# Kernel optimization log

Hardware: AMD Instinct MI355X
Metric: run time of the kernel (lower is better)

The kernel has to match this reference:

```python
import jax, jax.numpy as jnp
import numpy as np

# dims
N, NPG, E, D, ED = 32768, 256, 262144, 128, 32   # nodes, nodes/graph, edges, hidden, edge_dim
HG, CG = 4, 32                                    # GAT heads, per-head channels (HG*CG == D)
HA = 8                                            # global attention heads
DH = D // HA


def _glorot(key, shape):
    fan_in, fan_out = shape[0], shape[-1]
    lim = (6.0 / (fan_in + fan_out)) ** 0.5
    return jax.random.uniform(key, shape, jnp.float32, -lim, lim)


def _ln(x, g, b, eps=1e-5):
    m = x.mean(-1, keepdims=True)
    v = ((x - m) ** 2).mean(-1, keepdims=True)
    return (x - m) * jax.lax.rsqrt(v + eps) * g + b


def setup_inputs() -> dict:
    key = jax.random.key(0)
    ks = jax.random.split(key, 32)
    x = jax.random.normal(ks[0], (N, D), jnp.float32)
    src = jax.random.randint(ks[1], (E,), 0, N, jnp.int32)
    # keep edges intra-graph (graphs are contiguous blocks of NPG nodes)
    dst = (src // NPG) * NPG + jax.random.randint(ks[2], (E,), 0, NPG, jnp.int32)
    edge_index = jnp.stack([src, dst])
    edge_attr = jax.random.normal(ks[3], (E, ED), jnp.float32)
    batch = (jnp.arange(N, dtype=jnp.int32) // NPG)
    return {
        "x": x, "edge_attr": edge_attr,
        # EdgeAwareGATv2 params
        "W_src": _glorot(ks[4], (D, HG * CG)), "W_dst": _glorot(ks[5], (D, HG * CG)),
        "W_edge": _glorot(ks[6], (ED, HG * CG)), "att": _glorot(ks[7], (1, HG, CG)),
        "gat_bias": jnp.zeros((HG * CG,), jnp.float32),
        # GraphMultiHeadAttention params
        "Wq": _glorot(ks[8], (D, D)), "bq": jnp.zeros((D,), jnp.float32),
        "Wk": _glorot(ks[9], (D, D)), "bk": jnp.zeros((D,), jnp.float32),
        "Wv": _glorot(ks[10], (D, D)), "bv": jnp.zeros((D,), jnp.float32),
        "Wo": _glorot(ks[11], (D, D)), "bo": jnp.zeros((D,), jnp.float32),
        "We": _glorot(ks[12], (ED, HA)), "be": jnp.zeros((HA,), jnp.float32),
        # block norms + FFN
        "ln1_g": jnp.ones((D,), jnp.float32), "ln1_b": jnp.zeros((D,), jnp.float32),
        "W1": _glorot(ks[13], (D, 2 * D)), "b1": jnp.zeros((2 * D,), jnp.float32),
        "W2": _glorot(ks[14], (2 * D, D)), "b2": jnp.zeros((D,), jnp.float32),
        "ln2_g": jnp.ones((D,), jnp.float32), "ln2_b": jnp.zeros((D,), jnp.float32),
        "edge_index": edge_index, "batch": batch, "nodes_per_graph": NPG,
    }


def reference(x, edge_attr, W_src, W_dst, W_edge, att, gat_bias,
              Wq, bq, Wk, bk, Wv, bv, Wo, bo, We, be,
              ln1_g, ln1_b, W1, b1, W2, b2, ln2_g, ln2_b,
              edge_index, batch, nodes_per_graph):
    n = int(nodes_per_graph)
    Nn = x.shape[0]
    G = Nn // n
    src, dst = edge_index[0], edge_index[1]

    # ---- local: EdgeAwareGATv2 (segment-softmax attention over incoming edges) ----
    xs = (x @ W_src).reshape(Nn, HG, CG)
    xd = (x @ W_dst).reshape(Nn, HG, CG)
    ef = (edge_attr @ W_edge).reshape(-1, HG, CG)
    msg = jnp.tanh(xs[src] + xd[dst] + ef)                 # [E,HG,CG]
    alpha = (msg * att).sum(-1)                            # [E,HG]
    amax = jax.ops.segment_max(alpha, dst, num_segments=Nn)
    amax = jnp.where(jnp.isfinite(amax), amax, 0.0)        # nodes w/o in-edges
    ex = jnp.exp(alpha - amax[dst])
    den = jax.ops.segment_sum(ex, dst, num_segments=Nn)
    a = ex / (den[dst] + 1e-16)
    h_local = jax.ops.segment_sum(xs[src] * a[:, :, None], dst, num_segments=Nn)
    h_local = h_local.reshape(Nn, HG * CG) + gat_bias

    # ---- global: GraphMultiHeadAttention with edge bias (dense per graph) ----
    q = (x @ Wq + bq).reshape(G, n, HA, DH)
    k = (x @ Wk + bk).reshape(G, n, HA, DH)
    v = (x @ Wv + bv).reshape(G, n, HA, DH)
    attn = jnp.einsum('gnhd,gmhd->gnmh', q, k) * (DH ** -0.5)
    eb = edge_attr @ We + be                               # [E,HA]
    g_id = src // n
    intra = (g_id == dst // n)[:, None]
    attn = attn.at[g_id, src % n, dst % n].add(jnp.where(intra, eb, 0.0))
    attn = jax.nn.softmax(attn, axis=2)                    # softmax over keys (torch dim=1)
    h_attn = jnp.einsum('gnmh,gmhd->gnhd', attn, v).reshape(Nn, D)
    h_attn = h_attn @ Wo + bo

    # ---- GPS combine: residual + norm + FFN ----
    h = _ln(x + h_local + h_attn, ln1_g, ln1_b)
    ffn = jax.nn.gelu(h @ W1 + b1, approximate=False) @ W2 + b2
    return _ln(h + ffn, ln2_g, ln2_b)
```

## Files before the change

### kernel.cpp

```cpp
#include <hip/hip_runtime.h>
#include <hip/hip_bf16.h>

typedef __hip_bfloat16 bf16;
typedef __hip_bfloat162 bf162;
typedef __attribute__((ext_vector_type(8))) short short8;
typedef __attribute__((ext_vector_type(4))) float f32x4;
typedef __attribute__((ext_vector_type(16))) float f32x16;

constexpr int kN   = 32768;
constexpr int kG   = 128;
constexpr int kE   = 262144;
constexpr int kHA  = 8;

__device__ __forceinline__ float b2f(bf16 v){ return __bfloat162float(v); }
__device__ __forceinline__ bf16  f2b(float v){ return __float2bfloat16(v); }
__device__ __forceinline__ float b2f_raw(unsigned short u){
  return __uint_as_float((unsigned)u << 16);
}
__device__ __forceinline__ float tanh_fast(float x){
  float e = __expf(2.f*x);
  return 1.f - 2.f/(e+1.f);
}
__device__ __forceinline__ unsigned int cvtpk_bf16(float lo, float hi){
  unsigned int r;
  asm volatile("v_cvt_pk_bf16_f32 %0, %1, %2" : "=v"(r) : "v"(lo), "v"(hi));
  return r;
}
__device__ __forceinline__ void plane_swap(unsigned int &a, unsigned int &b){
  asm volatile("v_permlane32_swap_b32 %0, %1" : "+v"(a), "+v"(b));
}

__global__ void detect_k(const void* xraw, int* flag){
  const bf16* p = (const bf16*)xraw;
  int good = 0;
  for (int i = threadIdx.x; i < 4096; i += 256){
    float v = fabsf(b2f(p[i]));
    if (v > 0.0009765625f && v < 16.f) good++;
  }
  __shared__ int s[256];
  s[threadIdx.x] = good;
  __syncthreads();
  for (int d = 128; d; d >>= 1){
    if (threadIdx.x < d) s[threadIdx.x] += s[threadIdx.x + d];
    __syncthreads();
  }
  if (threadIdx.x == 0) *flag = (s[0] < 3500) ? 1 : 0;
}

struct ImpEnt { const void* src; void* dst; int n; };
struct ImpArgs { ImpEnt e[23]; };
__global__ __launch_bounds__(256) void import_k(ImpArgs a, const int* __restrict__ flag){
  ImpEnt en = a.e[blockIdx.y];
  const bool f32 = (*flag != 0);
  for (int i = blockIdx.x*256 + threadIdx.x; i < en.n; i += gridDim.x*256){
    float v = f32 ? ((const float*)en.src)[i] : b2f(((const bf16*)en.src)[i]);
    ((float*)en.dst)[i] = v;
  }
}

__global__ __launch_bounds__(256) void repack5_k(const float* __restrict__ W0,
    const float* __restrict__ W1p, const float* __restrict__ W2p,
    const float* __restrict__ W3p, const float* __restrict__ W4p,
    bf16* __restrict__ dst){
  int idx = blockIdx.x*256 + threadIdx.x;
  const float* Ws[5] = {W0, W1p, W2p, W3p, W4p};
  int o = idx >> 14;
  int rem = idx & 16383;
  int j = rem & 7, l = (rem >> 3) & 63, t = rem >> 9;
  int ks = t >> 3, cb = t & 7;
  int k = ks*32 + (l>>4)*8 + j;
  int c = cb*16 + (l&15);
  dst[idx] = f2b(Ws[o][k*128 + c]);
}

struct RepEnt { const float* src; bf16* dst; int total; int ncb_log; int dout; int mode; };
__global__ __launch_bounds__(256) void repack_k(RepEnt e0, RepEnt e1, RepEnt e2,
                                                RepEnt e3, RepEnt e4){
  RepEnt en = (blockIdx.y == 0) ? e0 : (blockIdx.y == 1) ? e1 :
              (blockIdx.y == 2) ? e2 : (blockIdx.y == 3) ? e3 : e4;
  int idx = blockIdx.x*256 + threadIdx.x;
  if (idx >= en.total) return;
  int j = idx & 7, l = (idx >> 3) & 63, t = idx >> 9;
  if (en.mode == 2){
    int k = (l>>4)*8 + j;
    int c = l & 15;
    en.dst[idx] = (c < 8) ? f2b(en.src[k*8 + c]) : f2b(0.f);
    return;
  }
  int ncbm = (1 << en.ncb_log) - 1;
  int ks = t >> en.ncb_log, cb = t & ncbm;
  int k = ks*32 + (l>>4)*8 + j;
  int c = cb*16 + (l&15);
  if (en.mode == 1) c = ((c & 15) << 3) | (c >> 4);
  en.dst[idx] = f2b(en.src[k*en.dout + c]);
}

__global__ __launch_bounds__(256) void gemm5_k(const void* __restrict__ xraw,
    const int* __restrict__ flag,
    const bf16* __restrict__ Wrep, const float* __restrict__ bias5,
    bf16* __restrict__ proj5){
  const int tid = threadIdx.x;
  const int wid = tid >> 6, l = tid & 63;
  const long r0 = (long)blockIdx.x*64 + wid*16;
  const bool f32 = (*flag != 0);
  short8 af[4];
  if (f32){
    const float* fr = (const float*)xraw + (r0 + (l&15))*128;
    #pragma unroll
    for (int ks=0; ks<4; ks++){
      float4 a = *(const float4*)(fr + ks*32 + (l>>4)*8);
      float4 b = *(const float4*)(fr + ks*32 + (l>>4)*8 + 4);
      union{ unsigned int u[4]; short8 s; } c;
      c.u[0]=cvtpk_bf16(a.x,a.y); c.u[1]=cvtpk_bf16(a.z,a.w);
      c.u[2]=cvtpk_bf16(b.x,b.y); c.u[3]=cvtpk_bf16(b.z,b.w);
      af[ks] = c.s;
    }
  } else {
    const short* Arow = (const short*)xraw + (r0 + (l&15))*128;
    #pragma unroll
    for (int ks=0; ks<4; ks++)
      af[ks] = *(const short8*)(Arow + ks*32 + (l>>4)*8);
  }
  const short8* Wp = (const short8*)Wrep;
  const int cc = l & 15, rr = (l >> 4) * 4;
  #pragma unroll 1
  for (int o=0; o<5; o++){
    f32x4 acc[8];
    #pragma unroll
    for (int cb=0; cb<8; cb++) acc[cb] = (f32x4){0.f,0.f,0.f,0.f};
    #pragma unroll
    for (int ks=0; ks<4; ks++){
      #pragma unroll
      for (int cb=0; cb<8; cb++){
        short8 bf = Wp[(o*32 + ks*8 + cb)*64 + l];
        acc[cb] = __builtin_amdgcn_mfma_f32_16x16x32_bf16(af[ks], bf, acc[cb], 0,0,0);
      }
    }
    bf16* outb = proj5 + (long)o*kN*128;
    #pragma unroll
    for (int cb=0; cb<8; cb++){
      float bb = bias5[o*128 + cb*16 + cc];
      #pragma unroll
      for (int r=0; r<4; r++){
        long row = r0 + rr + r;
        outb[row*128 + cb*16 + cc] = f2b(acc[cb][r] + bb);
      }
    }
  }
}

template<int DIN, int DOUT, int EPI>
__global__ __launch_bounds__(256) void gemm_mfma_k(const bf16* __restrict__ A,
    const bf16* __restrict__ Wrep, const float* __restrict__ bias,
    bf16* __restrict__ C){
  constexpr int KS = DIN/32, NCB = DOUT/16;
  const int tid = threadIdx.x;
  const int wid = tid >> 6, l = tid & 63;
  const long r0 = (long)blockIdx.x*64 + wid*16;
  const short* Arow = (const short*)(A + (r0 + (l&15))*(long)DIN);
  short8 af[KS];
  #pragma unroll
  for (int ks=0; ks<KS; ks++)
    af[ks] = *(const short8*)(Arow + ks*32 + (l>>4)*8);
  f32x4 acc[NCB];
  #pragma unroll
  for (int cb=0; cb<NCB; cb++) acc[cb] = (f32x4){0.f,0.f,0.f,0.f};
  const short8* Wp = (const short8*)Wrep;
  #pragma unroll
  for (int ks=0; ks<KS; ks++){
    #pragma unroll
    for (int cb=0; cb<NCB; cb++){
      short8 bf = Wp[(ks*NCB + cb)*64 + l];
      acc[cb] = __builtin_amdgcn_mfma_f32_16x16x32_bf16(af[ks], bf, acc[cb], 0,0,0);
    }
  }
  const int cc = l & 15, rr = (l >> 4) * 4;
  #pragma unroll
  for (int cb=0; cb<NCB; cb++){
    float bb = bias[cb*16 + cc];
    #pragma unroll
    for (int r=0; r<4; r++){
      long row = r0 + rr + r;
      float v = acc[cb][r] + bb;
      if (EPI == 2) v = 0.5f*v*(1.f + erff(v*0.70710678118654752f));
      C[row*DOUT + cb*16 + cc] = f2b(v);
    }
  }
}

__global__ void hist_k(const int* __restrict__ dstA, int* __restrict__ cnt){
  int e = blockIdx.x*256 + threadIdx.x;
  if (e < kE) atomicAdd(&cnt[dstA[e]], 1);
}

__global__ __launch_bounds__(1024) void scan_k(const int* __restrict__ cnt, int* __restrict__ rowptr){
  __shared__ int part[1024];
  const int t = threadIdx.x;
  const int base = t*32;
  int s = 0;
  #pragma unroll
  for (int i=0;i<32;i++) s += cnt[base+i];
  part[t] = s;
  __syncthreads();
  for (int d=1; d<1024; d<<=1){
    int v = (t>=d) ? part[t-d] : 0;
    __syncthreads();
    part[t] += v;
    __syncthreads();
  }
  int run = (t==0) ? 0 : part[t-1];
  for (int i=0;i<32;i++){ rowptr[base+i] = run; run += cnt[base+i]; }
  if (t == 1023) rowptr[kN] = run;
}

__global__ void scatter_k(const int* __restrict__ dstA, const int* __restrict__ rowptr,
                          int* __restrict__ cursor, int* __restrict__ eidx){
  int e = blockIdx.x*256 + threadIdx.x;
  if (e < kE){
    int d = dstA[e];
    int p = atomicAdd(&cursor[d], 1);
    eidx[rowptr[d]+p] = e;
  }
}

__global__ __launch_bounds__(256) void edge3_k(const void* __restrict__ ea_raw,
    const int* __restrict__ flag,
    const int* __restrict__ eidx, const int* __restrict__ srcA,
    const int* __restrict__ dstA,
    const bf16* __restrict__ xs, const bf16* __restrict__ xd,
    const bf16* __restrict__ WeR_edge,
    const bf16* __restrict__ WeR_eb,
    const float* __restrict__ att_f, const float* __restrict__ be_f,
    float* __restrict__ expal_t, float* __restrict__ ebuf_t,
    unsigned short* __restrict__ epack, int* __restrict__ src_t){
  __shared__ int sEid[64], sSrc[64], sDst[64];
  __shared__ float sAlphaF[64*4];
  const int tid = threadIdx.x;
  const int w = tid >> 6, l = tid & 63;
  const int p = blockIdx.x;
  const int bid = (p & 7) * (gridDim.x >> 3) + (p >> 3);
  const long t0 = (long)bid * 64;
  const bool f32 = (*flag != 0);

  if (tid < 64){
    int e = eidx[t0 + tid];
    int s = srcA[e], d = dstA[e];
    sEid[tid] = e; sSrc[tid] = s; sDst[tid] = d;
    src_t[t0 + tid] = s;
    epack[t0 + tid] = (unsigned short)(((s & 255) << 8) | (d & 255));
  }
  __syncthreads();

  short8 af;
  {
    long eoff = (long)sEid[w*16 + (l&15)]*32 + (l>>4)*8;
    if (f32){
      const float* er = (const float*)ea_raw + eoff;
      float4 a = *(const float4*)er;
      float4 b = *(const float4*)(er + 4);
      union{ unsigned int u[4]; short8 s; } c;
      c.u[0]=cvtpk_bf16(a.x,a.y); c.u[1]=cvtpk_bf16(a.z,a.w);
      c.u[2]=cvtpk_bf16(b.x,b.y); c.u[3]=cvtpk_bf16(b.z,b.w);
      af = c.s;
    } else {
      af = *(const short8*)((const short*)ea_raw + eoff);
    }
  }

  f32x4 acc[8], acc_eb;
  #pragma unroll
  for (int cb=0; cb<8; cb++){
    short8 wb = *(const short8*)((const short*)WeR_edge + (cb*64 + l)*8);
    acc[cb] = __builtin_amdgcn_mfma_f32_16x16x32_bf16(af, wb,
                (f32x4){0.f,0.f,0.f,0.f}, 0,0,0);
  }
  {
    short8 wbe = *(const short8*)((const short*)WeR_eb + l*8);
    acc_eb = __builtin_amdgcn_mfma_f32_16x16x32_bf16(af, wbe,
                (f32x4){0.f,0.f,0.f,0.f}, 0,0,0);
  }

  const int c15 = l & 15;
  const float be_v = be_f[c15 & 7];
  float4 at0 = *(const float4*)(att_f + c15*8);
  float4 at1 = *(const float4*)(att_f + c15*8 + 4);
  const float attv[8] = {at0.x,at0.y,at0.z,at0.w, at1.x,at1.y,at1.z,at1.w};
  union U8 { short8 s8; unsigned short u[8]; };
  U8 gx[4], gd[4];
  #pragma unroll
  for (int r=0; r<4; r++){
    int e_l = w*16 + (l>>4)*4 + r;
    gx[r].s8 = *(const short8*)((const short*)xs + (long)sSrc[e_l]*128 + c15*8);
    gd[r].s8 = *(const short8*)((const short*)xd + (long)sDst[e_l]*128 + c15*8);
  }
  #pragma unroll
  for (int r=0; r<4; r++){
    int e_l = w*16 + (l>>4)*4 + r;
    float hsum = 0.f;
    #pragma unroll
    for (int cb=0; cb<8; cb++){
      float v = acc[cb][r] + b2f_raw(gx[r].u[cb]) + b2f_raw(gd[r].u[cb]);
      hsum += tanh_fast(v) * attv[cb];
    }
    hsum += __shfl_xor(hsum,1);
    hsum += __shfl_xor(hsum,2);
    if ((c15 & 3) == 0) sAlphaF[e_l*4 + (c15>>2)] = __expf(hsum);
    if (c15 < 8) ebuf_t[(long)c15*kE + t0 + e_l] = acc_eb[r] + be_v;
  }
  __syncthreads();
  if (tid < 64)
    *(float4*)&expal_t[(t0 + tid)*4] = *(float4*)&sAlphaF[tid*4];
}

__global__ __launch_bounds__(256) void gat_agg_k(const float* __restrict__ expal,
    const int* __restrict__ rowptr, const int* __restrict__ src_t,
    const bf16* __restrict__ xs, const float* __restrict__ gatb_f,
    bf16* __restrict__ h_local){
  const int tid = threadIdx.x;
  const int grp = tid >> 5;
  const int l   = tid & 31;
  const int p   = blockIdx.x;
  const int bid = (p & 7) * (gridDim.x >> 3) + (p >> 3);
  const int v   = bid*8 + grp;
  const int c0  = l*4;
  const int head = l >> 3;
  const int beg = rowptr[v], end = rowptr[v+1];
  float den = 0.f, o0 = 0.f, o1 = 0.f, o2 = 0.f, o3 = 0.f;
  const unsigned short* xsu = (const unsigned short*)xs;
  for (int t = beg; t < end; t++){
    float w = expal[(long)t*4 + head];
    long s = src_t[t];
    ushort4 a = *(const ushort4*)(xsu + s*128 + c0);
    den += w;
    o0 += w*b2f_raw(a.x); o1 += w*b2f_raw(a.y);
    o2 += w*b2f_raw(a.z); o3 += w*b2f_raw(a.w);
  }
  float inv = 1.f/(den + 1e-16f);
  float4 gb = *(const float4*)(gatb_f + c0);
  unsigned int lo = cvtpk_bf16(o0*inv + gb.x, o1*inv + gb.y);
  unsigned int hi = cvtpk_bf16(o2*inv + gb.z, o3*inv + gb.w);
  *(uint2*)&((unsigned short*)h_local)[(long)v*128 + c0] = (uint2){lo, hi};
}

__global__ __launch_bounds__(512, 6) void attn2_k(const bf16* __restrict__ qb,
    const bf16* __restrict__ kb, const bf16* __restrict__ vb,
    const float* __restrict__ ebuf_t, const unsigned short* __restrict__ epack,
    const int* __restrict__ rowptr, bf16* __restrict__ hattn){
  __shared__ short Vf[16*64*8];
  __shared__ float sb[256*33];
  const int bid = blockIdx.x;
  const int h = (bid >> 3) >> 4;
  const int g = (((bid >> 3) & 15) << 3) | (bid & 7);
  const int tid = threadIdx.x;
  const int w = tid >> 6, l = tid & 63;
  const int q31 = l & 31, hi = l >> 5;
  const int nbase = g << 8;

  for (int s2 = tid; s2 < 1024; s2 += 512){
    int f = s2 >> 6, ll = s2 & 63;
    int keyb = (f>>1)*32 + (f&1)*16 + ((ll>>5)*8);
    int d = ll & 15;
    short tmp[8];
    #pragma unroll
    for (int j=0;j<8;j++)
      tmp[j] = ((const short*)vb)[((long)(nbase + keyb + j))*128 + h*16 + d];
    *(short8*)&Vf[s2*8] = *(short8*)tmp;
  }
  for (int i = tid; i < 256*33; i += 512) sb[i] = 0.f;
  short8 qf = *(const short8*)((const short*)qb + ((long)(nbase + w*32 + q31))*128 + h*16 + hi*8);
  __syncthreads();

  float m = -1e30f, lsum = 0.f;
  f32x16 oacc = {0.f,0.f,0.f,0.f,0.f,0.f,0.f,0.f,0.f,0.f,0.f,0.f,0.f,0.f,0.f,0.f};
  #pragma unroll 1
  for (int kt = 0; kt < 8; kt++){
    int rb = rowptr[nbase + kt*32];
    int re = rowptr[nbase + kt*32 + 32];
    for (int t = rb + tid; t < re; t += 512){
      unsigned int p = epack[t];
      atomicAdd(&sb[(p>>8)*33 + (p&31)], ebuf_t[(long)h*kE + t]);
    }
    __syncthreads();
    short8 af = *(const short8*)((const short*)kb +
                 ((long)(nbase + kt*32 + q31))*128 + h*16 + hi*8);
    f32x16 acc = {0.f,0.f,0.f,0.f,0.f,0.f,0.f,0.f,0.f,0.f,0.f,0.f,0.f,0.f,0.f,0.f};
    acc = __builtin_amdgcn_mfma_f32_32x32x16_bf16(af, qf, acc, 0, 0, 0);
    float s[16];
    float* brow = &sb[(w*32 + q31)*33];
    #pragma unroll
    for (int r=0;r<16;r++){
      int krow = (r&3) + 8*(r>>2) + 4*hi;
      s[r] = acc[r]*0.25f + brow[krow];
      brow[krow] = 0.f;
    }
    __syncthreads();
    float tmax = s[0];
    #pragma unroll
    for (int r=1;r<16;r++) tmax = fmaxf(tmax, s[r]);
    tmax = fmaxf(tmax, __shfl_xor(tmax, 32));
    float mn = fmaxf(m, tmax);
    float corrq = __expf(m - mn);
    m = mn;
    float psum = 0.f;
    #pragma unroll
    for (int r=0;r<16;r++){ s[r] = __expf(s[r] - m); psum += s[r]; }
    lsum = lsum*corrq + psum;
    #pragma unroll
    for (int r=0;r<16;r++){
      int qrow = (r&3) + 8*(r>>2) + 4*hi;
      oacc[r] *= __shfl(corrq, qrow);
    }
    unsigned int a  = cvtpk_bf16(s[0],  s[1]);
    unsigned int b  = cvtpk_bf16(s[2],  s[3]);
    unsigned int c  = cvtpk_bf16(s[4],  s[5]);
    unsigned int d  = cvtpk_bf16(s[6],  s[7]);
    unsigned int e  = cvtpk_bf16(s[8],  s[9]);
    unsigned int f  = cvtpk_bf16(s[10], s[11]);
    unsigned int g2 = cvtpk_bf16(s[12], s[13]);
    unsigned int h2 = cvtpk_bf16(s[14], s[15]);
    plane_swap(a, c); plane_swap(b, d); plane_swap(e, g2); plane_swap(f, h2);
    union { unsigned int u[4]; short8 s8; } A1, A2;
    A1.u[0]=a; A1.u[1]=b; A1.u[2]=c; A1.u[3]=d;
    A2.u[0]=e; A2.u[1]=f; A2.u[2]=g2; A2.u[3]=h2;
    short8 v1 = *(short8*)&Vf[((kt*2+0)*64 + l)*8];
    short8 v2 = *(short8*)&Vf[((kt*2+1)*64 + l)*8];
    oacc = __builtin_amdgcn_mfma_f32_32x32x16_bf16(A1.s8, v1, oacc, 0,0,0);
    oacc = __builtin_amdgcn_mfma_f32_32x32x16_bf16(A2.s8, v2, oacc, 0,0,0);
  }
  lsum += __shfl_xor(lsum, 32);
  float linv = 1.f / lsum;
  #pragma unroll
  for (int r=0;r<16;r++){
    int qrow = (r&3) + 8*(r>>2) + 4*hi;
    float li = __shfl(linv, qrow);
    float ov = oacc[r]*li;
    if (q31 < 16)
      hattn[((long)(nbase + w*32 + qrow))*128 + h*16 + q31] = f2b(ov);
  }
}

__global__ __launch_bounds__(256) void combine_ln_k(const void* __restrict__ a,
    const bf16* __restrict__ b, const bf16* __restrict__ c3,
    const float* __restrict__ g, const float* __restrict__ bb,
    void* __restrict__ outp, const int* __restrict__ flag,
    int a_raw, int is_final){
  const int tid = threadIdx.x;
  const int lane = tid & 63;
  const long row = (long)blockIdx.x*4 + (tid>>6);
  const long base = row*128;
  float a0, a1;
  if (a_raw && (*flag)){
    const float* ap = (const float*)a;
    a0 = ap[base+lane]; a1 = ap[base+lane+64];
  } else {
    const bf16* ap = (const bf16*)a;
    a0 = b2f(ap[base+lane]); a1 = b2f(ap[base+lane+64]);
  }
  float v0 = a0 + b2f(b[base+lane]);
  float v1 = a1 + b2f(b[base+lane+64]);
  if (c3){ v0 += b2f(c3[base+lane]); v1 += b2f(c3[base+lane+64]); }
  float s = v0 + v1;
  #pragma unroll
  for (int o=1; o<64; o<<=1) s += __shfl_xor(s, o);
  float mean = s * (1.f/128.f);
  float d0 = v0 - mean, d1 = v1 - mean;
  float q = d0*d0 + d1*d1;
  #pragma unroll
  for (int o=1; o<64; o<<=1) q += __shfl_xor(q, o);
  float r = rsqrtf(q*(1.f/128.f) + 1e-5f);
  float r0v = d0*r*g[lane]    + bb[lane];
  float r1v = d1*r*g[lane+64] + bb[lane+64];
  if (is_final && (*flag)){
    float* o = (float*)outp;
    o[base+lane]    = r0v;
    o[base+lane+64] = r1v;
  } else {
    bf16* o = (bf16*)outp;
    o[base+lane]    = f2b(r0v);
    o[base+lane+64] = f2b(r1v);
  }
}

extern "C" void kernel_launch(void* const* d_in, const int* in_sizes, int n_in,
                              void* d_out, int out_size, void* d_ws, size_t ws_size,
                              hipStream_t stream){
  const void* x_raw   = d_in[0];
  const void* ea_raw  = d_in[1];
  const int*  ei      = (const int*)d_in[25];
  const int* srcA = ei;
  const int* dstA = ei + kE;

  char* ws = (char*)d_ws;
  size_t off = 0;
  auto alloc = [&](size_t bytes)->void*{
    void* p = ws + off;
    off = (off + bytes + 255) & ~(size_t)255;
    return p;
  };
  int*   flag    = (int*)alloc(4);
  float* Wsrc_f  = (float*)alloc(16384*4);
  float* Wdst_f  = (float*)alloc(16384*4);
  float* Wedge_f = (float*)alloc(4096*4);
  float* att_f   = (float*)alloc(128*4);
  float* gatb_f  = (float*)alloc(128*4);
  float* Wq_f    = (float*)alloc(16384*4);
  float* Wk_f    = (float*)alloc(16384*4);
  float* Wv_f    = (float*)alloc(16384*4);
  float* Wo_f    = (float*)alloc(16384*4);
  float* bo_f    = (float*)alloc(128*4);
  float* We_f    = (float*)alloc(256*4);
  float* be_f    = (float*)alloc(8*4);
  float* ln1g_f  = (float*)alloc(128*4);
  float* ln1b_f  = (float*)alloc(128*4);
  float* W1_f    = (float*)alloc(32768*4);
  float* b1_f    = (float*)alloc(256*4);
  float* W2_f    = (float*)alloc(32768*4);
  float* b2_f    = (float*)alloc(128*4);
  float* ln2g_f  = (float*)alloc(128*4);
  float* ln2b_f  = (float*)alloc(128*4);
  float* bias5   = (float*)alloc(640*4);
  bf16*  Wrep5   = (bf16*)alloc((size_t)5*16384*2);
  bf16*  WoR     = (bf16*)alloc((size_t)16384*2);
  bf16*  W1R     = (bf16*)alloc((size_t)32768*2);
  bf16*  W2R     = (bf16*)alloc((size_t)32768*2);
  bf16*  WeR     = (bf16*)alloc((size_t)4096*2);
  bf16*  WeRb    = (bf16*)alloc((size_t)512*2);
  bf16*  proj5   = (bf16*)alloc((size_t)5*kN*128*2);
  bf16* xs   = proj5;
  bf16* xd   = proj5 + (size_t)kN*128;
  bf16* qb   = proj5 + (size_t)2*kN*128;
  bf16* kbuf = proj5 + (size_t)3*kN*128;
  bf16* vbuf = proj5 + (size_t)4*kN*128;
  int* cnt        = (int*)alloc((size_t)2*kN*4);
  int* cursor     = cnt + kN;
  int* rowptr     = (int*)alloc((size_t)(kN+1)*4);
  int* eidx       = (int*)alloc((size_t)kE*4);
  unsigned short* epack = (unsigned short*)alloc((size_t)kE*2);
  float* ebuf_t   = (float*)alloc((size_t)8*kE*4);
  float* expal_t  = (float*)alloc((size_t)kE*4*4);
  int*   src_t    = (int*)alloc((size_t)kE*4);
  bf16* h_local   = (bf16*)alloc((size_t)kN*128*2);
  bf16* hattn_pre = (bf16*)alloc((size_t)kN*128*2);
  bf16* h_attn    = (bf16*)alloc((size_t)kN*128*2);
  bf16* hbuf      = (bf16*)alloc((size_t)kN*128*2);
  bf16* tbuf      = (bf16*)alloc((size_t)kN*256*2);
  bf16* f2buf     = (bf16*)alloc((size_t)kN*128*2);
  (void)ws_size; (void)in_sizes; (void)n_in; (void)out_size;

  dim3 b256(256);

  detect_k<<<1, b256, 0, stream>>>(x_raw, flag);
  hipMemsetAsync(bias5, 0, 256*4, stream);
  hipMemsetAsync(cnt, 0, (size_t)2*kN*4, stream);

  hist_k<<<kE/256, b256, 0, stream>>>(dstA, cnt);
  scan_k<<<1, 1024, 0, stream>>>(cnt, rowptr);
  scatter_k<<<kE/256, b256, 0, stream>>>(dstA, rowptr, cursor, eidx);

  ImpArgs ia;
  const void* srcs[23] = {d_in[2], d_in[3], d_in[4], d_in[5], d_in[6],
                          d_in[7], d_in[8], d_in[9], d_in[10], d_in[11], d_in[12],
                          d_in[13], d_in[14], d_in[15], d_in[16], d_in[17], d_in[18],
                          d_in[19], d_in[20], d_in[21], d_in[22], d_in[23], d_in[24]};
  void* dsts[23] = {Wsrc_f, Wdst_f, Wedge_f, att_f, gatb_f,
                    Wq_f, bias5+256, Wk_f, bias5+384, Wv_f, bias5+512,
                    Wo_f, bo_f, We_f, be_f, ln1g_f, ln1b_f,
                    W1_f, b1_f, W2_f, b2_f, ln2g_f, ln2b_f};
  int ns[23] = {16384, 16384, 4096, 128, 128,
                16384, 128, 16384, 128, 16384, 128,
                16384, 128, 256, 8, 128, 128,
                32768, 256, 32768, 128, 128, 128};
  for (int i=0;i<23;i++){ ia.e[i].src=srcs[i]; ia.e[i].dst=dsts[i]; ia.e[i].n=ns[i]; }
  import_k<<<dim3(64,23), b256, 0, stream>>>(ia, flag);

  repack5_k<<<(5*16384)/256, b256, 0, stream>>>(Wsrc_f, Wdst_f, Wq_f, Wk_f, Wv_f, Wrep5);
  RepEnt ro{Wo_f, WoR, 16384, 3, 128, 0};
  RepEnt r1{W1_f, W1R, 32768, 4, 256, 0};
  RepEnt r2{W2_f, W2R, 32768, 3, 128, 0};
  RepEnt re{Wedge_f, WeR, 4096, 3, 128, 1};
  RepEnt rb{We_f, WeRb, 512, 0, 8, 2};
  repack_k<<<dim3(128,5), b256, 0, stream>>>(ro, r1, r2, re, rb);

  gemm5_k<<<kN/64, b256, 0, stream>>>(x_raw, flag, Wrep5, bias5, proj5);

  edge3_k<<<kE/64, b256, 0, stream>>>(ea_raw, flag, eidx, srcA, dstA, xs, xd,
                                      WeR, WeRb, att_f, be_f,
                                      expal_t, ebuf_t, epack, src_t);

  gat_agg_k<<<kN/8, b256, 0, stream>>>(expal_t, rowptr, src_t, xs, gatb_f, h_local);

  attn2_k<<<kG*kHA, dim3(512), 0, stream>>>(qb, kbuf, vbuf, ebuf_t, epack, rowptr, hattn_pre);
  gemm_mfma_k<128,128,1><<<kN/64, b256, 0, stream>>>(hattn_pre, WoR, bo_f, h_attn);

  combine_ln_k<<<kN/4, b256, 0, stream>>>(x_raw, h_local, h_attn, ln1g_f, ln1b_f,
                                          hbuf, flag, 1, 0);

  gemm_mfma_k<128,256,2><<<kN/64, b256, 0, stream>>>(hbuf, W1R, b1_f, tbuf);
  gemm_mfma_k<256,128,1><<<kN/64, b256, 0, stream>>>(tbuf, W2R, b2_f, f2buf);

  combine_ln_k<<<kN/4, b256, 0, stream>>>(hbuf, f2buf, nullptr, ln2g_f, ln2b_f,
                                          d_out, flag, 0, 1);
}
```

Measured before the change: 234.9 us.

## Build source-sorted CSR for edge bias and drop shared-memory atomic bias tiles

Adds a second CSR keyed by source node (histogram, scan, scatter) that packs each edge's dst-local key and its dst-sorted position. The attention kernel now has each query lane walk its own source edge list to add edge bias into registers. This replaces the shared-memory bias tile, its LDS atomics and two barriers per key tile. It also drops the online-softmax running max and rescaling, exponentiating raw scores directly. That adds three preprocessing kernels and rescans each query's edge list eight times, and removing max subtraction risks overflow when scores are large.

After: 339.9 us. 44.7% more time.

```diff
diff --git a/kernel.cpp b/kernel.cpp
--- a/kernel.cpp
+++ b/kernel.cpp
@@ -188,9 +188,9 @@
   }
 }
 
-__global__ void hist_k(const int* __restrict__ dstA, int* __restrict__ cnt){
+__global__ void hist_k(const int* __restrict__ idxA, int* __restrict__ cnt){
   int e = blockIdx.x*256 + threadIdx.x;
-  if (e < kE) atomicAdd(&cnt[dstA[e]], 1);
+  if (e < kE) atomicAdd(&cnt[idxA[e]], 1);
 }
 
 __global__ __launch_bounds__(1024) void scan_k(const int* __restrict__ cnt, int* __restrict__ rowptr){
@@ -214,12 +214,26 @@
 }
 
 __global__ void scatter_k(const int* __restrict__ dstA, const int* __restrict__ rowptr,
-                          int* __restrict__ cursor, int* __restrict__ eidx){
+                          int* __restrict__ cursor, int* __restrict__ eidx,
+                          int* __restrict__ pos_t){
   int e = blockIdx.x*256 + threadIdx.x;
   if (e < kE){
     int d = dstA[e];
     int p = atomicAdd(&cursor[d], 1);
-    eidx[rowptr[d]+p] = e;
+    int t = rowptr[d]+p;
+    eidx[t] = e;
+    pos_t[e] = t;
+  }
+}
+
+__global__ void scatter2_k(const int* __restrict__ srcA, const int* __restrict__ dstA,
+                           const int* __restrict__ srcptr, int* __restrict__ cursor2,
+                           const int* __restrict__ pos_t, unsigned int* __restrict__ packed){
+  int e = blockIdx.x*256 + threadIdx.x;
+  if (e < kE){
+    int s = srcA[e];
+    int p = atomicAdd(&cursor2[s], 1);
+    packed[srcptr[s]+p] = ((unsigned int)(dstA[e] & 255) << 24) | (unsigned int)pos_t[e];
   }
 }
 
@@ -232,7 +246,7 @@
     const bf16* __restrict__ WeR_eb,
     const float* __restrict__ att_f, const float* __restrict__ be_f,
     float* __restrict__ expal_t, float* __restrict__ ebuf_t,
-    unsigned short* __restrict__ epack, int* __restrict__ src_t){
+    int* __restrict__ src_t){
   __shared__ int sEid[64], sSrc[64], sDst[64];
   __shared__ float sAlphaF[64*4];
   const int tid = threadIdx.x;
@@ -247,7 +261,6 @@
     int s = srcA[e], d = dstA[e];
     sEid[tid] = e; sSrc[tid] = s; sDst[tid] = d;
     src_t[t0 + tid] = s;
-    epack[t0 + tid] = (unsigned short)(((s & 255) << 8) | (d & 255));
   }
   __syncthreads();
 
@@ -342,12 +355,11 @@
   *(uint2*)&((unsigned short*)h_local)[(long)v*128 + c0] = (uint2){lo, hi};
 }
 
-__global__ __launch_bounds__(512, 6) void attn2_k(const bf16* __restrict__ qb,
+__global__ __launch_bounds__(512, 6) void attn3_k(const bf16* __restrict__ qb,
     const bf16* __restrict__ kb, const bf16* __restrict__ vb,
-    const float* __restrict__ ebuf_t, const unsigned short* __restrict__ epack,
-    const int* __restrict__ rowptr, bf16* __restrict__ hattn){
+    const float* __restrict__ ebuf_t, const int* __restrict__ srcptr,
+    const unsigned int* __restrict__ packed, bf16* __restrict__ hattn){
   __shared__ short Vf[16*64*8];
-  __shared__ float sb[256*33];
   const int bid = blockIdx.x;
   const int h = (bid >> 3) >> 4;
   const int g = (((bid >> 3) & 15) << 3) | (bid & 7);
@@ -366,50 +378,44 @@
       tmp[j] = ((const short*)vb)[((long)(nbase + keyb + j))*128 + h*16 + d];
     *(short8*)&Vf[s2*8] = *(short8*)tmp;
   }
-  for (int i = tid; i < 256*33; i += 512) sb[i] = 0.f;
   short8 qf = *(const short8*)((const short*)qb + ((long)(nbase + w*32 + q31))*128 + h*16 + hi*8);
+  const int q = nbase + w*32 + q31;
+  const int u0 = srcptr[q], u1 = srcptr[q+1];
+  const float* ebh = ebuf_t + (long)h*kE;
   __syncthreads();
 
-  float m = -1e30f, lsum = 0.f;
+  float lsum = 0.f;
   f32x16 oacc = {0.f,0.f,0.f,0.f,0.f,0.f,0.f,0.f,0.f,0.f,0.f,0.f,0.f,0.f,0.f,0.f};
+  short8 kf = *(const short8*)((const short*)kb + ((long)(nbase + q31))*128 + h*16 + hi*8);
   #pragma unroll 1
   for (int kt = 0; kt < 8; kt++){
-    int rb = rowptr[nbase + kt*32];
-    int re = rowptr[nbase + kt*32 + 32];
-    for (int t = rb + tid; t < re; t += 512){
-      unsigned int p = epack[t];
-      atomicAdd(&sb[(p>>8)*33 + (p&31)], ebuf_t[(long)h*kE + t]);
-    }
-    __syncthreads();
-    short8 af = *(const short8*)((const short*)kb +
-                 ((long)(nbase + kt*32 + q31))*128 + h*16 + hi*8);
+    short8 kcur = kf;
+    if (kt < 7)
+      kf = *(const short8*)((const short*)kb +
+            ((long)(nbase + (kt+1)*32 + q31))*128 + h*16 + hi*8);
     f32x16 acc = {0.f,0.f,0.f,0.f,0.f,0.f,0.f,0.f,0.f,0.f,0.f,0.f,0.f,0.f,0.f,0.f};
-    acc = __builtin_amdgcn_mfma_f32_32x32x16_bf16(af, qf, acc, 0, 0, 0);
+    acc = __builtin_amdgcn_mfma_f32_32x32x16_bf16(kcur, qf, acc, 0, 0, 0);
+    float badd[16];
+    #pragma unroll
+    for (int rr=0;rr<16;rr++) badd[rr] = 0.f;
+    for (int u = u0; u < u1; ++u){
+      unsigned int v = packed[u];
+      unsigned int key = v >> 24;
+      if ((int)(key >> 5) == kt && (int)((key >> 2) & 1) == hi){
+        int re = (int)(key & 3) | ((int)((key & 31) >> 3) << 2);
+        float b = ebh[v & 0xFFFFFFu];
+        #pragma unroll
+        for (int rr=0;rr<16;rr++) badd[rr] += (rr == re) ? b : 0.f;
+      }
+    }
     float s[16];
-    float* brow = &sb[(w*32 + q31)*33];
+    float psum = 0.f;
     #pragma unroll
     for (int r=0;r<16;r++){
-      int krow = (r&3) + 8*(r>>2) + 4*hi;
-      s[r] = acc[r]*0.25f + brow[krow];
-      brow[krow] = 0.f;
-    }
-    __syncthreads();
-    float tmax = s[0];
-    #pragma unroll
-    for (int r=1;r<16;r++) tmax = fmaxf(tmax, s[r]);
-    tmax = fmaxf(tmax, __shfl_xor(tmax, 32));
-    float mn = fmaxf(m, tmax);
-    float corrq = __expf(m - mn);
-    m = mn;
-    float psum = 0.f;
-    #pragma unroll
-    for (int r=0;r<16;r++){ s[r] = __expf(s[r] - m); psum += s[r]; }
-    lsum = lsum*corrq + psum;
-    #pragma unroll
-    for (int r=0;r<16;r++){
-      int qrow = (r&3) + 8*(r>>2) + 4*hi;
-      oacc[r] *= __shfl(corrq, qrow);
-    }
+      s[r] = __expf(fmaf(acc[r], 0.25f, badd[r]));
+      psum += s[r];
+    }
+    lsum += psum;
     unsigned int a  = cvtpk_bf16(s[0],  s[1]);
     unsigned int b  = cvtpk_bf16(s[2],  s[3]);
     unsigned int c  = cvtpk_bf16(s[4],  s[5]);
@@ -531,11 +537,15 @@
   bf16* qb   = proj5 + (size_t)2*kN*128;
   bf16* kbuf = proj5 + (size_t)3*kN*128;
   bf16* vbuf = proj5 + (size_t)4*kN*128;
-  int* cnt        = (int*)alloc((size_t)2*kN*4);
+  int* cnt        = (int*)alloc((size_t)4*kN*4);
   int* cursor     = cnt + kN;
+  int* cnt2       = cnt + 2*kN;
+  int* cursor2    = cnt + 3*kN;
   int* rowptr     = (int*)alloc((size_t)(kN+1)*4);
+  int* srcptr     = (int*)alloc((size_t)(kN+1)*4);
   int* eidx       = (int*)alloc((size_t)kE*4);
-  unsigned short* epack = (unsigned short*)alloc((size_t)kE*2);
+  int* pos_t      = (int*)alloc((size_t)kE*4);
+  unsigned int* packed = (unsigned int*)alloc((size_t)kE*4);
   float* ebuf_t   = (float*)alloc((size_t)8*kE*4);
   float* expal_t  = (float*)alloc((size_t)kE*4*4);
   int*   src_t    = (int*)alloc((size_t)kE*4);
@@ -551,11 +561,14 @@
 
   detect_k<<<1, b256, 0, stream>>>(x_raw, flag);
   hipMemsetAsync(bias5, 0, 256*4, stream);
-  hipMemsetAsync(cnt, 0, (size_t)2*kN*4, stream);
+  hipMemsetAsync(cnt, 0, (size_t)4*kN*4, stream);
 
   hist_k<<<kE/256, b256, 0, stream>>>(dstA, cnt);
   scan_k<<<1, 1024, 0, stream>>>(cnt, rowptr);
-  scatter_k<<<kE/256, b256, 0, stream>>>(dstA, rowptr, cursor, eidx);
+  scatter_k<<<kE/256, b256, 0, stream>>>(dstA, rowptr, cursor, eidx, pos_t);
+  hist_k<<<kE/256, b256, 0, stream>>>(srcA, cnt2);
+  scan_k<<<1, 1024, 0, stream>>>(cnt2, srcptr);
+  scatter2_k<<<kE/256, b256, 0, stream>>>(srcA, dstA, srcptr, cursor2, pos_t, packed);
 
   ImpArgs ia;
   const void* srcs[23] = {d_in[2], d_in[3], d_in[4], d_in[5], d_in[6],
@@ -585,11 +598,11 @@
 
   edge3_k<<<kE/64, b256, 0, stream>>>(ea_raw, flag, eidx, srcA, dstA, xs, xd,
                                       WeR, WeRb, att_f, be_f,
-                                      expal_t, ebuf_t, epack, src_t);
+                                      expal_t, ebuf_t, src_t);
 
   gat_agg_k<<<kN/8, b256, 0, stream>>>(expal_t, rowptr, src_t, xs, gatb_f, h_local);
 
-  attn2_k<<<kG*kHA, dim3(512), 0, stream>>>(qb, kbuf, vbuf, ebuf_t, epack, rowptr, hattn_pre);
+  attn3_k<<<kG*kHA, dim3(512), 0, stream>>>(qb, kbuf, vbuf, ebuf_t, srcptr, packed, hattn_pre);
   gemm_mfma_k<128,128,1><<<kN/64, b256, 0, stream>>>(hattn_pre, WoR, bo_f, h_attn);
 
   combine_ln_k<<<kN/4, b256, 0, stream>>>(x_raw, h_local, h_attn, ln1g_f, ln1b_f,
```
